# Performance work log

Measured on AMD Instinct MI355X. Metric: run time of the kernel, lower is better.

The kernel has to match this reference:

```python
import jax, jax.numpy as jnp
import numpy as np

EPS = 1e-7  # keras.backend.epsilon()


def _squash(x):
    # Original applies squash over the trailing size-1 axis of [B,N,1,D,1],
    # so the squared 'norm' is just x**2 elementwise. Faithful reproduction.
    sq = jnp.square(x)
    scale = sq / (1.0 + sq) / jnp.sqrt(sq + EPS)
    return scale * x


def setup_inputs() -> dict:
    key = jax.random.key(0)
    k1, k2, k3 = jax.random.split(key, 3)
    B, N, I, D, Din = 64, 32, 1152, 16, 8
    x = jax.random.normal(k1, (B, I, Din), dtype=jnp.float32)
    # W init: random_normal(mean=0, stddev=1)
    W = jax.random.normal(k2, (N, I, D, Din), dtype=jnp.float32)
    dense_w = jax.random.normal(k3, (1, 1), dtype=jnp.float32) * 0.05
    dense_b = jnp.zeros((1,), dtype=jnp.float32)
    return {"x": x, "W": W, "dense_w": dense_w, "dense_b": dense_b}


def reference(x, W, dense_w, dense_b, routings=3):
    # u_hat[b,n,i,d] = sum_k W[n,i,d,k] * x[b,i,k]   (the tf.map_fn batched matmul)
    u_hat = jnp.einsum('nidk,bik->bnid', W, x)  # [B,N,I,D]
    B, N, I, D = u_hat.shape
    b = jnp.zeros((B, N, I), dtype=u_hat.dtype)
    v = None
    for it in range(routings):
        c = jax.nn.softmax(b, axis=1)                 # softmax over output capsules N
        s = jnp.einsum('bni,bnid->bnd', c, u_hat)     # weighted sum over input caps I
        v = _squash(s)                                # [B,N,D] (elementwise squash quirk)
        if it < routings - 1:
            b = b + jnp.einsum('bnid,bnd->bni', u_hat, v)  # agreement update
    # v_j squeezed -> [B,N,D,1]; Dense(1, sigmoid) on the trailing size-1 axis
    out = jax.nn.sigmoid(jnp.matmul(v[..., None], dense_w) + dense_b)  # [B,N,D,1]
    return out
```

## Files before the change

kernel.cpp:

```cpp
#include <hip/hip_runtime.h>

constexpr int B_ = 64, N_ = 32, I_ = 1152, D_ = 16, K_ = 8;
constexpr int SVD = B_ * N_ * D_;

template <int MODE, int NIC>
__global__ __launch_bounds__(256, 2) void route7(
    const float* __restrict__ W, const float* __restrict__ x,
    const float* __restrict__ veff, float* __restrict__ partial)
{
    constexpr int ICLEN = I_ / NIC;
    __shared__ __align__(16) float wlds[2][4096];

    int bid = blockIdx.x;
    int ic, bg;
    if constexpr ((NIC & 7) == 0) {
        constexpr int icpx = NIC / 8;
        int x8 = bid & 7, r = bid >> 3;
        ic = x8 * icpx + (r % icpx);
        bg = r / icpx;
    } else { ic = bid >> 2; bg = bid & 3; }

    const int tid = threadIdx.x;
    const int w = tid >> 6, l = tid & 63;
    const int n = l & 31, dh = l >> 5, d0 = dh * 8;
    const int bB = bg * 16 + w * 4;
    const int i0 = ic * ICLEN;

    float ve[4][8];
    if constexpr (MODE == 1) {
#pragma unroll
        for (int bb = 0; bb < 4; ++bb) {
            const float* vp = veff + ((bB + bb) * N_ + n) * D_ + d0;
            float4 a = *(const float4*)vp, b = *(const float4*)(vp + 4);
            ve[bb][0] = a.x;  ve[bb][1] = a.y;  ve[bb][2] = a.z;  ve[bb][3] = a.w;
            ve[bb][4] = b.x;  ve[bb][5] = b.y;  ve[bb][6] = b.z;  ve[bb][7] = b.w;
        }
    }

    const int nsl = tid >> 3, p0 = tid & 7;
    const float* wrow = W + (size_t)nsl * (I_ * D_ * K_) + (size_t)i0 * 128;

    float sacc[4][8];
#pragma unroll
    for (int bb = 0; bb < 4; ++bb)
#pragma unroll
        for (int j = 0; j < 8; ++j) sacc[bb][j] = 0.f;

    float4 st[4];
    auto stage_load = [&](int t) {
#pragma unroll
        for (int r = 0; r < 4; ++r)
            st[r] = *(const float4*)(wrow + (size_t)t * 128 + (p0 + 8 * r) * 4);
    };
    auto stage_write = [&](int buf) {
#pragma unroll
        for (int r = 0; r < 4; ++r) {
            int g = p0 + 8 * r;
            *(float4*)&wlds[buf][nsl * 128 + ((g + nsl) & 31) * 4] = st[r];
        }
    };

    stage_load(0);
    stage_write(0);

    for (int t = 0; t < ICLEN; ++t) {
        __syncthreads();
        if (t + 1 < ICLEN) stage_load(t + 1);
        const int buf = t & 1;
        const int i = i0 + t;

        float xr[4][8];
#pragma unroll
        for (int bb = 0; bb < 4; ++bb) {
            const float* xp = x + ((size_t)(bB + bb) * I_ + i) * K_;
            float4 a = *(const float4*)xp, c4 = *(const float4*)(xp + 4);
            xr[bb][0] = a.x;  xr[bb][1] = a.y;  xr[bb][2] = a.z;  xr[bb][3] = a.w;
            xr[bb][4] = c4.x; xr[bb][5] = c4.y; xr[bb][6] = c4.z; xr[bb][7] = c4.w;
        }

        float uh[4][8];
#pragma unroll
        for (int j = 0; j < 8; ++j) {
            int g0 = (d0 + j) * 2;
            float4 wa = *(const float4*)&wlds[buf][n * 128 + (((g0)     + n) & 31) * 4];
            float4 wb = *(const float4*)&wlds[buf][n * 128 + (((g0 + 1) + n) & 31) * 4];
#pragma unroll
            for (int bb = 0; bb < 4; ++bb) {
                float acc = wa.x * xr[bb][0] + wa.y * xr[bb][1] +
                            wa.z * xr[bb][2] + wa.w * xr[bb][3] +
                            wb.x * xr[bb][4] + wb.y * xr[bb][5] +
                            wb.z * xr[bb][6] + wb.w * xr[bb][7];
                if constexpr (MODE == 0) sacc[bb][j] += acc;
                else                     uh[bb][j] = acc;
            }
        }

        if constexpr (MODE == 1) {
#pragma unroll
            for (int bb = 0; bb < 4; ++bb) {
                float blp = 0.f;
#pragma unroll
                for (int j = 0; j < 8; ++j) blp += uh[bb][j] * ve[bb][j];
                blp += __shfl_xor(blp, 32);
                float mx = blp;
#pragma unroll
                for (int s2 = 16; s2 >= 1; s2 >>= 1) mx = fmaxf(mx, __shfl_xor(mx, s2));
                float e = __expf(blp - mx), sm = e;
#pragma unroll
                for (int s2 = 16; s2 >= 1; s2 >>= 1) sm += __shfl_xor(sm, s2);
                float c = e / sm;
#pragma unroll
                for (int j = 0; j < 8; ++j) sacc[bb][j] = fmaf(c, uh[bb][j], sacc[bb][j]);
            }
        }

        if (t + 1 < ICLEN) stage_write((t + 1) & 1);
    }

#pragma unroll
    for (int bb = 0; bb < 4; ++bb) {
        float* pb = partial + (size_t)ic * 32768 + (bB + bb) * 512 + n * 16 + d0;
        *(float4*)pb       = make_float4(sacc[bb][0], sacc[bb][1], sacc[bb][2], sacc[bb][3]);
        *(float4*)(pb + 4) = make_float4(sacc[bb][4], sacc[bb][5], sacc[bb][6], sacc[bb][7]);
    }
}

template <int RM, int NIC>
__global__ __launch_bounds__(256) void reduce7(
    const float* __restrict__ partial, float scale,
    const float* __restrict__ vprev, float* __restrict__ vout,
    const float* __restrict__ dw, const float* __restrict__ db,
    float* __restrict__ out)
{
    int e = blockIdx.x * 256 + threadIdx.x;
    float a0 = 0.f, a1 = 0.f, a2 = 0.f, a3 = 0.f;
    const float* p = partial + e;
#pragma unroll 2
    for (int q = 0; q + 4 <= NIC; q += 4) {
        a0 += p[(size_t)(q + 0) * 32768];
        a1 += p[(size_t)(q + 1) * 32768];
        a2 += p[(size_t)(q + 2) * 32768];
        a3 += p[(size_t)(q + 3) * 32768];
    }
    if constexpr (NIC & 3) {
        for (int q = NIC & ~3; q < NIC; ++q) a0 += p[(size_t)q * 32768];
    }
    float ss = ((a0 + a1) + (a2 + a3)) * scale;

    float sq = ss * ss;
    float sc = sq / (1.f + sq) / sqrtf(sq + 1e-7f);
    float v = sc * ss;
    if constexpr (RM == 0) {
        vout[e] = v;
    } else if constexpr (RM == 1) {
        vout[e] = vprev[e] + v;
    } else {
        float z = v * dw[0] + db[0];
        out[e] = 1.f / (1.f + __expf(-z));
    }
}

template <int NIC>
static void run_pipeline(const float* W, const float* x, const float* dw,
                         const float* db, float* out, void* d_ws, hipStream_t stream)
{
    float* partial = (float*)d_ws;
    float* vA = partial + (size_t)NIC * 32768;
    float* vB = vA + SVD;
    dim3 rblk(256), rgrid(NIC * 4), dgrid(SVD / 256);

    route7<0, NIC><<<rgrid, rblk, 0, stream>>>(W, x, nullptr, partial);
    reduce7<0, NIC><<<dgrid, rblk, 0, stream>>>(partial, 1.f / 32.f, nullptr, vA, nullptr, nullptr, nullptr);
    route7<1, NIC><<<rgrid, rblk, 0, stream>>>(W, x, vA, partial);
    reduce7<1, NIC><<<dgrid, rblk, 0, stream>>>(partial, 1.f, vA, vB, nullptr, nullptr, nullptr);
    route7<1, NIC><<<rgrid, rblk, 0, stream>>>(W, x, vB, partial);
    reduce7<2, NIC><<<dgrid, rblk, 0, stream>>>(partial, 1.f, nullptr, nullptr, dw, db, out);
}

extern "C" void kernel_launch(void* const* d_in, const int* in_sizes, int n_in,
                              void* d_out, int out_size, void* d_ws, size_t ws_size,
                              hipStream_t stream)
{
    const float* x  = (const float*)d_in[0];
    const float* W  = (const float*)d_in[1];
    const float* dw = (const float*)d_in[2];
    const float* db = (const float*)d_in[3];
    float* out = (float*)d_out;

    const size_t needMain = (size_t)192 * 32768 * 4 + 2ull * SVD * 4;
    if (ws_size >= needMain)
        run_pipeline<192>(W, x, dw, db, out, d_ws, stream);
    else
        run_pipeline<36>(W, x, dw, db, out, d_ws, stream);
}
```

Measured before the change: 159.6 us.

## Cut register pressure in routing kernel and raise occupancy and I-split count

Raises launch bounds from 2 to 4 blocks per SM. To fit that register budget, the kernel splits the K dimension into two halves of x loads, stops keeping veff resident in registers and reloads it per iteration, and packs two batch rows into one wave-wide softmax so the shuffle reductions cover two rows at once. It also raises the input-capsule split from 192 to 288 chunks, which adds more blocks but makes the partial buffer and the reduction pass larger. The risks are extra veff reloads from cache, register spills under the tighter bound, and more reduction traffic.

New measurement: 412.5 us. +158.4%, slower.

```diff
diff --git a/kernel.cpp b/kernel.cpp
--- a/kernel.cpp
+++ b/kernel.cpp
@@ -4,7 +4,7 @@
 constexpr int SVD = B_ * N_ * D_;
 
 template <int MODE, int NIC>
-__global__ __launch_bounds__(256, 2) void route7(
+__global__ __launch_bounds__(256, 4) void route9(
     const float* __restrict__ W, const float* __restrict__ x,
     const float* __restrict__ veff, float* __restrict__ partial)
 {
@@ -22,20 +22,9 @@
 
     const int tid = threadIdx.x;
     const int w = tid >> 6, l = tid & 63;
-    const int n = l & 31, dh = l >> 5, d0 = dh * 8;
+    const int n = l & 31, d0 = (l >> 5) * 8;
     const int bB = bg * 16 + w * 4;
     const int i0 = ic * ICLEN;
-
-    float ve[4][8];
-    if constexpr (MODE == 1) {
-#pragma unroll
-        for (int bb = 0; bb < 4; ++bb) {
-            const float* vp = veff + ((bB + bb) * N_ + n) * D_ + d0;
-            float4 a = *(const float4*)vp, b = *(const float4*)(vp + 4);
-            ve[bb][0] = a.x;  ve[bb][1] = a.y;  ve[bb][2] = a.z;  ve[bb][3] = a.w;
-            ve[bb][4] = b.x;  ve[bb][5] = b.y;  ve[bb][6] = b.z;  ve[bb][7] = b.w;
-        }
-    }
 
     const int nsl = tid >> 3, p0 = tid & 7;
     const float* wrow = W + (size_t)nsl * (I_ * D_ * K_) + (size_t)i0 * 128;
@@ -69,48 +58,69 @@
         const int buf = t & 1;
         const int i = i0 + t;
 
-        float xr[4][8];
-#pragma unroll
-        for (int bb = 0; bb < 4; ++bb) {
-            const float* xp = x + ((size_t)(bB + bb) * I_ + i) * K_;
-            float4 a = *(const float4*)xp, c4 = *(const float4*)(xp + 4);
-            xr[bb][0] = a.x;  xr[bb][1] = a.y;  xr[bb][2] = a.z;  xr[bb][3] = a.w;
-            xr[bb][4] = c4.x; xr[bb][5] = c4.y; xr[bb][6] = c4.z; xr[bb][7] = c4.w;
-        }
-
         float uh[4][8];
-#pragma unroll
-        for (int j = 0; j < 8; ++j) {
-            int g0 = (d0 + j) * 2;
-            float4 wa = *(const float4*)&wlds[buf][n * 128 + (((g0)     + n) & 31) * 4];
-            float4 wb = *(const float4*)&wlds[buf][n * 128 + (((g0 + 1) + n) & 31) * 4];
-#pragma unroll
-            for (int bb = 0; bb < 4; ++bb) {
-                float acc = wa.x * xr[bb][0] + wa.y * xr[bb][1] +
-                            wa.z * xr[bb][2] + wa.w * xr[bb][3] +
-                            wb.x * xr[bb][4] + wb.y * xr[bb][5] +
-                            wb.z * xr[bb][6] + wb.w * xr[bb][7];
-                if constexpr (MODE == 0) sacc[bb][j] += acc;
-                else                     uh[bb][j] = acc;
+        if constexpr (MODE == 1) {
+#pragma unroll
+            for (int bb = 0; bb < 4; ++bb)
+#pragma unroll
+                for (int j = 0; j < 8; ++j) uh[bb][j] = 0.f;
+        }
+
+#pragma unroll
+        for (int kh = 0; kh < 2; ++kh) {
+            float4 xv[4];
+#pragma unroll
+            for (int bb = 0; bb < 4; ++bb)
+                xv[bb] = *(const float4*)(x + ((size_t)(bB + bb) * I_ + i) * K_ + kh * 4);
+#pragma unroll
+            for (int j = 0; j < 8; ++j) {
+                int g = (d0 + j) * 2 + kh;
+                float4 wv = *(const float4*)&wlds[buf][n * 128 + ((g + n) & 31) * 4];
+#pragma unroll
+                for (int bb = 0; bb < 4; ++bb) {
+                    float acc = wv.x * xv[bb].x + wv.y * xv[bb].y +
+                                wv.z * xv[bb].z + wv.w * xv[bb].w;
+                    if constexpr (MODE == 0) sacc[bb][j] += acc;
+                    else                     uh[bb][j] += acc;
+                }
             }
         }
 
         if constexpr (MODE == 1) {
 #pragma unroll
-            for (int bb = 0; bb < 4; ++bb) {
-                float blp = 0.f;
-#pragma unroll
-                for (int j = 0; j < 8; ++j) blp += uh[bb][j] * ve[bb][j];
-                blp += __shfl_xor(blp, 32);
-                float mx = blp;
+            for (int p = 0; p < 2; ++p) {
+                const int b0i = 2 * p, b1i = 2 * p + 1;
+                const float* vp0 = veff + ((size_t)(bB + b0i) * N_ + n) * D_ + d0;
+                const float* vp1 = veff + ((size_t)(bB + b1i) * N_ + n) * D_ + d0;
+                float4 va0 = *(const float4*)vp0, vb0 = *(const float4*)(vp0 + 4);
+                float4 va1 = *(const float4*)vp1, vb1 = *(const float4*)(vp1 + 4);
+
+                float bl0 = va0.x * uh[b0i][0] + va0.y * uh[b0i][1] +
+                            va0.z * uh[b0i][2] + va0.w * uh[b0i][3] +
+                            vb0.x * uh[b0i][4] + vb0.y * uh[b0i][5] +
+                            vb0.z * uh[b0i][6] + vb0.w * uh[b0i][7];
+                float bl1 = va1.x * uh[b1i][0] + va1.y * uh[b1i][1] +
+                            va1.z * uh[b1i][2] + va1.w * uh[b1i][3] +
+                            vb1.x * uh[b1i][4] + vb1.y * uh[b1i][5] +
+                            vb1.z * uh[b1i][6] + vb1.w * uh[b1i][7];
+                bl0 += __shfl_xor(bl0, 32);
+                bl1 += __shfl_xor(bl1, 32);
+                float lp = (l < 32) ? bl0 : bl1;
+                float mx = lp;
 #pragma unroll
                 for (int s2 = 16; s2 >= 1; s2 >>= 1) mx = fmaxf(mx, __shfl_xor(mx, s2));
-                float e = __expf(blp - mx), sm = e;
+                float e = __expf(lp - mx), sm = e;
 #pragma unroll
                 for (int s2 = 16; s2 >= 1; s2 >>= 1) sm += __shfl_xor(sm, s2);
-                float c = e / sm;
-#pragma unroll
-                for (int j = 0; j < 8; ++j) sacc[bb][j] = fmaf(c, uh[bb][j], sacc[bb][j]);
+                float cp = e / sm;
+                float co = __shfl_xor(cp, 32);
+                float c0 = (l < 32) ? cp : co;
+                float c1 = (l < 32) ? co : cp;
+#pragma unroll
+                for (int j = 0; j < 8; ++j) {
+                    sacc[b0i][j] = fmaf(c0, uh[b0i][j], sacc[b0i][j]);
+                    sacc[b1i][j] = fmaf(c1, uh[b1i][j], sacc[b1i][j]);
+                }
             }
         }
 
@@ -126,7 +136,7 @@
 }
 
 template <int RM, int NIC>
-__global__ __launch_bounds__(256) void reduce7(
+__global__ __launch_bounds__(256) void reduce9(
     const float* __restrict__ partial, float scale,
     const float* __restrict__ vprev, float* __restrict__ vout,
     const float* __restrict__ dw, const float* __restrict__ db,
@@ -169,12 +179,12 @@
     float* vB = vA + SVD;
     dim3 rblk(256), rgrid(NIC * 4), dgrid(SVD / 256);
 
-    route7<0, NIC><<<rgrid, rblk, 0, stream>>>(W, x, nullptr, partial);
-    reduce7<0, NIC><<<dgrid, rblk, 0, stream>>>(partial, 1.f / 32.f, nullptr, vA, nullptr, nullptr, nullptr);
-    route7<1, NIC><<<rgrid, rblk, 0, stream>>>(W, x, vA, partial);
-    reduce7<1, NIC><<<dgrid, rblk, 0, stream>>>(partial, 1.f, vA, vB, nullptr, nullptr, nullptr);
-    route7<1, NIC><<<rgrid, rblk, 0, stream>>>(W, x, vB, partial);
-    reduce7<2, NIC><<<dgrid, rblk, 0, stream>>>(partial, 1.f, nullptr, nullptr, dw, db, out);
+    route9<0, NIC><<<rgrid, rblk, 0, stream>>>(W, x, nullptr, partial);
+    reduce9<0, NIC><<<dgrid, rblk, 0, stream>>>(partial, 1.f / 32.f, nullptr, vA, nullptr, nullptr, nullptr);
+    route9<1, NIC><<<rgrid, rblk, 0, stream>>>(W, x, vA, partial);
+    reduce9<1, NIC><<<dgrid, rblk, 0, stream>>>(partial, 1.f, vA, vB, nullptr, nullptr, nullptr);
+    route9<1, NIC><<<rgrid, rblk, 0, stream>>>(W, x, vB, partial);
+    reduce9<2, NIC><<<dgrid, rblk, 0, stream>>>(partial, 1.f, nullptr, nullptr, dw, db, out);
 }
 
 extern "C" void kernel_launch(void* const* d_in, const int* in_sizes, int n_in,
@@ -187,9 +197,9 @@
     const float* db = (const float*)d_in[3];
     float* out = (float*)d_out;
 
-    const size_t needMain = (size_t)192 * 32768 * 4 + 2ull * SVD * 4;
+    const size_t needMain = (size_t)288 * 32768 * 4 + 2ull * SVD * 4;
     if (ws_size >= needMain)
-        run_pipeline<192>(W, x, dw, db, out, d_ws, stream);
+        run_pipeline<288>(W, x, dw, db, out, d_ws, stream);
     else
         run_pipeline<36>(W, x, dw, db, out, d_ws, stream);
 }
```

## Pre-transpose W into lane-coalesced layout and drop LDS staging in routing kernel

Applied to the files above, without the earlier changes.

Adds a kernel that rearranges W once per call into a per-input-capsule layout, so each lane in the routing kernel can read its weights straight from global memory with coalesced float4 loads. The LDS double buffer and its per-iteration __syncthreads are removed. The routing softmax now handles two batch rows per wave pass, using lane-half selection, which halves the number of shuffle reductions. The trade-off is an extra full read and write of W (about 19 MB) on every call, plus the routing kernels relying on cache or HBM for weight reuse across blocks instead of shared memory.

After: 193.2 us. +21.0%, slower.

```diff
diff --git a/kernel.cpp b/kernel.cpp
--- a/kernel.cpp
+++ b/kernel.cpp
@@ -3,14 +3,30 @@
 constexpr int B_ = 64, N_ = 32, I_ = 1152, D_ = 16, K_ = 8;
 constexpr int SVD = B_ * N_ * D_;
 
+__global__ __launch_bounds__(256) void wtrans(const float* __restrict__ W,
+                                              float* __restrict__ Wt)
+{
+    int i = blockIdx.x;
+    int tid = threadIdx.x;
+    int n = tid >> 3, q = tid & 7;
+    const float* src = W + (size_t)n * (I_ * D_ * K_) + (size_t)i * 128 + q * 16;
+    float* dst = Wt + (size_t)i * 4096;
+#pragma unroll
+    for (int f = 0; f < 4; ++f) {
+        float4 v = *(const float4*)(src + f * 4);
+        int d = 2 * q + (f >> 1);
+        int p = (d & 7) * 2 + (f & 1);
+        int l = n + 32 * (d >> 3);
+        *(float4*)(dst + p * 256 + l * 4) = v;
+    }
+}
+
 template <int MODE, int NIC>
-__global__ __launch_bounds__(256, 2) void route7(
-    const float* __restrict__ W, const float* __restrict__ x,
+__global__ __launch_bounds__(256, 2) void routeT(
+    const float* __restrict__ Wt, const float* __restrict__ x,
     const float* __restrict__ veff, float* __restrict__ partial)
 {
     constexpr int ICLEN = I_ / NIC;
-    __shared__ __align__(16) float wlds[2][4096];
-
     int bid = blockIdx.x;
     int ic, bg;
     if constexpr ((NIC & 7) == 0) {
@@ -22,7 +38,7 @@
 
     const int tid = threadIdx.x;
     const int w = tid >> 6, l = tid & 63;
-    const int n = l & 31, dh = l >> 5, d0 = dh * 8;
+    const int n = l & 31, d0 = (l >> 5) * 8;
     const int bB = bg * 16 + w * 4;
     const int i0 = ic * ICLEN;
 
@@ -30,66 +46,44 @@
     if constexpr (MODE == 1) {
 #pragma unroll
         for (int bb = 0; bb < 4; ++bb) {
-            const float* vp = veff + ((bB + bb) * N_ + n) * D_ + d0;
+            const float* vp = veff + ((size_t)(bB + bb) * N_ + n) * D_ + d0;
             float4 a = *(const float4*)vp, b = *(const float4*)(vp + 4);
             ve[bb][0] = a.x;  ve[bb][1] = a.y;  ve[bb][2] = a.z;  ve[bb][3] = a.w;
             ve[bb][4] = b.x;  ve[bb][5] = b.y;  ve[bb][6] = b.z;  ve[bb][7] = b.w;
         }
     }
 
-    const int nsl = tid >> 3, p0 = tid & 7;
-    const float* wrow = W + (size_t)nsl * (I_ * D_ * K_) + (size_t)i0 * 128;
-
     float sacc[4][8];
 #pragma unroll
     for (int bb = 0; bb < 4; ++bb)
 #pragma unroll
         for (int j = 0; j < 8; ++j) sacc[bb][j] = 0.f;
 
-    float4 st[4];
-    auto stage_load = [&](int t) {
-#pragma unroll
-        for (int r = 0; r < 4; ++r)
-            st[r] = *(const float4*)(wrow + (size_t)t * 128 + (p0 + 8 * r) * 4);
-    };
-    auto stage_write = [&](int buf) {
-#pragma unroll
-        for (int r = 0; r < 4; ++r) {
-            int g = p0 + 8 * r;
-            *(float4*)&wlds[buf][nsl * 128 + ((g + nsl) & 31) * 4] = st[r];
-        }
-    };
-
-    stage_load(0);
-    stage_write(0);
+    const float* wl = Wt + (size_t)i0 * 4096 + l * 4;
 
     for (int t = 0; t < ICLEN; ++t) {
-        __syncthreads();
-        if (t + 1 < ICLEN) stage_load(t + 1);
-        const int buf = t & 1;
         const int i = i0 + t;
-
-        float xr[4][8];
+        const float* wi = wl + (size_t)t * 4096;
+
+        float4 xv[4][2];
 #pragma unroll
         for (int bb = 0; bb < 4; ++bb) {
             const float* xp = x + ((size_t)(bB + bb) * I_ + i) * K_;
-            float4 a = *(const float4*)xp, c4 = *(const float4*)(xp + 4);
-            xr[bb][0] = a.x;  xr[bb][1] = a.y;  xr[bb][2] = a.z;  xr[bb][3] = a.w;
-            xr[bb][4] = c4.x; xr[bb][5] = c4.y; xr[bb][6] = c4.z; xr[bb][7] = c4.w;
+            xv[bb][0] = *(const float4*)xp;
+            xv[bb][1] = *(const float4*)(xp + 4);
         }
 
         float uh[4][8];
 #pragma unroll
         for (int j = 0; j < 8; ++j) {
-            int g0 = (d0 + j) * 2;
-            float4 wa = *(const float4*)&wlds[buf][n * 128 + (((g0)     + n) & 31) * 4];
-            float4 wb = *(const float4*)&wlds[buf][n * 128 + (((g0 + 1) + n) & 31) * 4];
+            float4 w0 = *(const float4*)(wi + (j * 2    ) * 256);
+            float4 w1 = *(const float4*)(wi + (j * 2 + 1) * 256);
 #pragma unroll
             for (int bb = 0; bb < 4; ++bb) {
-                float acc = wa.x * xr[bb][0] + wa.y * xr[bb][1] +
-                            wa.z * xr[bb][2] + wa.w * xr[bb][3] +
-                            wb.x * xr[bb][4] + wb.y * xr[bb][5] +
-                            wb.z * xr[bb][6] + wb.w * xr[bb][7];
+                float acc = w0.x * xv[bb][0].x + w0.y * xv[bb][0].y +
+                            w0.z * xv[bb][0].z + w0.w * xv[bb][0].w +
+                            w1.x * xv[bb][1].x + w1.y * xv[bb][1].y +
+                            w1.z * xv[bb][1].z + w1.w * xv[bb][1].w;
                 if constexpr (MODE == 0) sacc[bb][j] += acc;
                 else                     uh[bb][j] = acc;
             }
@@ -97,24 +91,34 @@
 
         if constexpr (MODE == 1) {
 #pragma unroll
-            for (int bb = 0; bb < 4; ++bb) {
-                float blp = 0.f;
-#pragma unroll
-                for (int j = 0; j < 8; ++j) blp += uh[bb][j] * ve[bb][j];
-                blp += __shfl_xor(blp, 32);
-                float mx = blp;
+            for (int p2 = 0; p2 < 2; ++p2) {
+                const int b0i = 2 * p2, b1i = 2 * p2 + 1;
+                float bl0 = 0.f, bl1 = 0.f;
+#pragma unroll
+                for (int j = 0; j < 8; ++j) {
+                    bl0 += uh[b0i][j] * ve[b0i][j];
+                    bl1 += uh[b1i][j] * ve[b1i][j];
+                }
+                bl0 += __shfl_xor(bl0, 32);
+                bl1 += __shfl_xor(bl1, 32);
+                float lp = (l < 32) ? bl0 : bl1;
+                float mx = lp;
 #pragma unroll
                 for (int s2 = 16; s2 >= 1; s2 >>= 1) mx = fmaxf(mx, __shfl_xor(mx, s2));
-                float e = __expf(blp - mx), sm = e;
+                float e = __expf(lp - mx), sm = e;
 #pragma unroll
                 for (int s2 = 16; s2 >= 1; s2 >>= 1) sm += __shfl_xor(sm, s2);
-                float c = e / sm;
-#pragma unroll
-                for (int j = 0; j < 8; ++j) sacc[bb][j] = fmaf(c, uh[bb][j], sacc[bb][j]);
+                float cp = e / sm;
+                float co = __shfl_xor(cp, 32);
+                float c0 = (l < 32) ? cp : co;
+                float c1 = (l < 32) ? co : cp;
+#pragma unroll
+                for (int j = 0; j < 8; ++j) {
+                    sacc[b0i][j] = fmaf(c0, uh[b0i][j], sacc[b0i][j]);
+                    sacc[b1i][j] = fmaf(c1, uh[b1i][j], sacc[b1i][j]);
+                }
             }
         }
-
-        if (t + 1 < ICLEN) stage_write((t + 1) & 1);
     }
 
 #pragma unroll
@@ -126,7 +130,7 @@
 }
 
 template <int RM, int NIC>
-__global__ __launch_bounds__(256) void reduce7(
+__global__ __launch_bounds__(256) void reduceT(
     const float* __restrict__ partial, float scale,
     const float* __restrict__ vprev, float* __restrict__ vout,
     const float* __restrict__ dw, const float* __restrict__ db,
@@ -164,17 +168,19 @@
 static void run_pipeline(const float* W, const float* x, const float* dw,
                          const float* db, float* out, void* d_ws, hipStream_t stream)
 {
-    float* partial = (float*)d_ws;
+    float* Wt = (float*)d_ws;
+    float* partial = Wt + (size_t)I_ * 4096;
     float* vA = partial + (size_t)NIC * 32768;
     float* vB = vA + SVD;
     dim3 rblk(256), rgrid(NIC * 4), dgrid(SVD / 256);
 
-    route7<0, NIC><<<rgrid, rblk, 0, stream>>>(W, x, nullptr, partial);
-    reduce7<0, NIC><<<dgrid, rblk, 0, stream>>>(partial, 1.f / 32.f, nullptr, vA, nullptr, nullptr, nullptr);
-    route7<1, NIC><<<rgrid, rblk, 0, stream>>>(W, x, vA, partial);
-    reduce7<1, NIC><<<dgrid, rblk, 0, stream>>>(partial, 1.f, vA, vB, nullptr, nullptr, nullptr);
-    route7<1, NIC><<<rgrid, rblk, 0, stream>>>(W, x, vB, partial);
-    reduce7<2, NIC><<<dgrid, rblk, 0, stream>>>(partial, 1.f, nullptr, nullptr, dw, db, out);
+    wtrans<<<I_, 256, 0, stream>>>(W, Wt);
+    routeT<0, NIC><<<rgrid, rblk, 0, stream>>>(Wt, x, nullptr, partial);
+    reduceT<0, NIC><<<dgrid, rblk, 0, stream>>>(partial, 1.f / 32.f, nullptr, vA, nullptr, nullptr, nullptr);
+    routeT<1, NIC><<<rgrid, rblk, 0, stream>>>(Wt, x, vA, partial);
+    reduceT<1, NIC><<<dgrid, rblk, 0, stream>>>(partial, 1.f, vA, vB, nullptr, nullptr, nullptr);
+    routeT<1, NIC><<<rgrid, rblk, 0, stream>>>(Wt, x, vB, partial);
+    reduceT<2, NIC><<<dgrid, rblk, 0, stream>>>(partial, 1.f, nullptr, nullptr, dw, db, out);
 }
 
 extern "C" void kernel_launch(void* const* d_in, const int* in_sizes, int n_in,
@@ -187,9 +193,13 @@
     const float* db = (const float*)d_in[3];
     float* out = (float*)d_out;
 
-    const size_t needMain = (size_t)192 * 32768 * 4 + 2ull * SVD * 4;
-    if (ws_size >= needMain)
+    const size_t wtB = (size_t)I_ * 4096 * 4;
+    const size_t need192 = wtB + (size_t)192 * 32768 * 4 + 2ull * SVD * 4;
+    const size_t need36  = wtB + (size_t)36  * 32768 * 4 + 2ull * SVD * 4;
+    if (ws_size >= need192)
         run_pipeline<192>(W, x, dw, db, out, d_ws, stream);
+    else if (ws_size >= need36)
+        run_pipeline<36>(W, x, dw, db, out, d_ws, stream);
     else
-        run_pipeline<36>(W, x, dw, db, out, d_ws, stream);
-}
+        run_pipeline<4>(W, x, dw, db, out, d_ws, stream);
+}
```
